# Kernel tuning notes

Hardware: AMD Instinct MI355X
Metric: run time of the kernel (lower is better)

The kernel has to match this reference:

```python
import jax, jax.numpy as jnp
import numpy as np

IN_CH = 512
MID_CH = IN_CH // 8  # 64


def setup_inputs() -> dict:
    key = jax.random.key(0)
    ks = jax.random.split(key, 7)
    B, C, H, W = 8, IN_CH, 64, 64
    s = 1.0 / np.sqrt(C)
    x = jax.random.normal(ks[0], (B, C, H, W), dtype=jnp.float32)
    wq = jax.random.normal(ks[1], (MID_CH, C), dtype=jnp.float32) * s
    bq = jax.random.normal(ks[2], (MID_CH,), dtype=jnp.float32) * 0.01
    wk = jax.random.normal(ks[3], (MID_CH, C), dtype=jnp.float32) * s
    bk = jax.random.normal(ks[4], (MID_CH,), dtype=jnp.float32) * 0.01
    wv = jax.random.normal(ks[5], (C, C), dtype=jnp.float32) * s
    bv = jax.random.normal(ks[6], (C,), dtype=jnp.float32) * 0.01
    gamma = jnp.array([0.5], dtype=jnp.float32)
    return {"x": x, "wq": wq, "bq": bq, "wk": wk, "bk": bk,
            "wv": wv, "bv": bv, "gamma": gamma}


def reference(x, wq, bq, wk, bk, wv, bv, gamma):
    B, C, H, W = x.shape
    N = H * W
    xf = x.reshape(B, C, N)  # flatten spatial -> [B, C, N]
    # 1x1 convs are channel-wise matmuls
    q = jnp.einsum('mc,bcn->bnm', wq, xf) + bq  # [B, N, mid]
    k = jnp.einsum('mc,bcn->bmn', wk, xf) + bk[None, :, None]  # [B, mid, N]
    v = jnp.einsum('oc,bcn->bon', wv, xf) + bv[None, :, None]  # [B, C, N]
    sim = jnp.einsum('bnm,bmj->bnj', q, k)  # [B, N, N]
    sim = jax.nn.softmax(sim, axis=-1)
    # feat[b,c,i] = sum_j v[b,c,j] * sim[b,i,j]   (value @ sim^T)
    feat = jnp.einsum('bcj,bij->bci', v, sim).reshape(B, C, H, W)
    return gamma[0] * feat + x
```

## Files before the change

kernel.cpp:

```cpp
#include <hip/hip_runtime.h>
#include <hip/hip_bf16.h>


#define BB 8
#define CC 512
#define MM 64
#define NN 4096
#define LOG2E 1.4426950408889634f

typedef __attribute__((ext_vector_type(8))) short bf16x8;
typedef __attribute__((ext_vector_type(8))) _Float16 f16x8;
typedef __attribute__((ext_vector_type(4))) float f32x4;

__device__ unsigned g_kmax[BB];

__device__ __forceinline__ unsigned short f2bf(float f) {
  union { float f; unsigned u; } v; v.f = f;
  unsigned r = v.u + 0x7fffu + ((v.u >> 16) & 1u);
  return (unsigned short)(r >> 16);
}
__device__ __forceinline__ float bf2f(unsigned short h) {
  union { unsigned u; float f; } v; v.u = ((unsigned)h) << 16;
  return v.f;
}
__device__ __forceinline__ unsigned short f2h(float f) {
  union { _Float16 h; unsigned short u; } v; v.h = (_Float16)f;
  return v.u;
}

__global__ __launch_bounds__(256) void k_wconv(
    const float* __restrict__ wq, const float* __restrict__ wk,
    const float* __restrict__ wv,
    unsigned short* __restrict__ wqhi, unsigned short* __restrict__ wqlo,
    unsigned short* __restrict__ wkhi, unsigned short* __restrict__ wklo,
    unsigned short* __restrict__ wvbf) {
  const int tid = blockIdx.x * 256 + threadIdx.x;
  if (tid < BB) g_kmax[tid] = 0u;
  if (tid < MM * CC) {
    float v = wq[tid];
    unsigned short h = f2bf(v);
    wqhi[tid] = h; wqlo[tid] = f2bf(v - bf2f(h));
    v = wk[tid]; h = f2bf(v);
    wkhi[tid] = h; wklo[tid] = f2bf(v - bf2f(h));
  }
  for (int i = tid; i < CC * CC; i += 65536) wvbf[i] = f2bf(wv[i]);
}

__global__ __launch_bounds__(256) void k_transpose(const float* __restrict__ x,
                                                   unsigned short* __restrict__ xT) {
  __shared__ float tile[64][65];
  const int b = blockIdx.z, c0 = blockIdx.y * 64, n0 = blockIdx.x * 64;
  const int t = threadIdx.x;
  {
    const int nl = t & 63, cl0 = t >> 6;
    const float* xp = x + ((size_t)b * CC + c0) * NN + n0;
#pragma unroll
    for (int r = 0; r < 16; r++) {
      const int cl = cl0 + r * 4;
      tile[cl][nl] = xp[(size_t)cl * NN + nl];
    }
  }
  __syncthreads();
  {
    const int cl = t & 63, nl0 = t >> 6;
    unsigned short* xtp = xT + ((size_t)b * NN + n0) * CC + c0;
#pragma unroll
    for (int r = 0; r < 16; r++) {
      const int nl = nl0 + r * 4;
      xtp[(size_t)nl * CC + cl] = f2bf(tile[cl][nl]);
    }
  }
}

__global__ __launch_bounds__(256, 2) void k_proj(
    const unsigned short* __restrict__ xT,
    const unsigned short* __restrict__ wqhi, const unsigned short* __restrict__ wqlo,
    const unsigned short* __restrict__ wkhi, const unsigned short* __restrict__ wklo,
    const float* __restrict__ bq, const float* __restrict__ bk,
    const unsigned short* __restrict__ wvbf, const float* __restrict__ bv,
    unsigned short* __restrict__ qf, unsigned short* __restrict__ kf,
    unsigned short* __restrict__ vbf) {
  __shared__ float ksl[4][4][16];
  const int t = threadIdx.x, w = t >> 6, l = t & 63, lr = l & 15, g = l >> 4;

  if (blockIdx.x < 512) {
    const int b = blockIdx.x & 7;
    const int n0 = (blockIdx.x >> 3) * 64;
    const unsigned short* qhp = wqhi + (size_t)(w * 16 + lr) * CC + g * 8;
    const unsigned short* qlp = wqlo + (size_t)(w * 16 + lr) * CC + g * 8;
    const unsigned short* khp = wkhi + (size_t)(w * 16 + lr) * CC + g * 8;
    const unsigned short* klp = wklo + (size_t)(w * 16 + lr) * CC + g * 8;
    const unsigned short* xp = xT + ((size_t)b * NN + n0 + lr) * CC + g * 8;
    f32x4 qacc[4], kacc[4];
#pragma unroll
    for (int nf = 0; nf < 4; nf++) {
      qacc[nf] = f32x4{0.f, 0.f, 0.f, 0.f};
      kacc[nf] = f32x4{0.f, 0.f, 0.f, 0.f};
    }
    for (int cc = 0; cc < CC; cc += 32) {
      const bf16x8 qh8 = *reinterpret_cast<const bf16x8*>(qhp + cc);
      const bf16x8 ql8 = *reinterpret_cast<const bf16x8*>(qlp + cc);
      const bf16x8 kh8 = *reinterpret_cast<const bf16x8*>(khp + cc);
      const bf16x8 kl8 = *reinterpret_cast<const bf16x8*>(klp + cc);
      bf16x8 xb[4];
#pragma unroll
      for (int nf = 0; nf < 4; nf++)
        xb[nf] = *reinterpret_cast<const bf16x8*>(xp + (size_t)nf * 16 * CC + cc);
#pragma unroll
      for (int nf = 0; nf < 4; nf++) {
        qacc[nf] = __builtin_amdgcn_mfma_f32_16x16x32_bf16(qh8, xb[nf], qacc[nf], 0, 0, 0);
        qacc[nf] = __builtin_amdgcn_mfma_f32_16x16x32_bf16(ql8, xb[nf], qacc[nf], 0, 0, 0);
        kacc[nf] = __builtin_amdgcn_mfma_f32_16x16x32_bf16(kh8, xb[nf], kacc[nf], 0, 0, 0);
        kacc[nf] = __builtin_amdgcn_mfma_f32_16x16x32_bf16(kl8, xb[nf], kacc[nf], 0, 0, 0);
      }
    }
    float bqv[4], bkv[4];
#pragma unroll
    for (int r = 0; r < 4; r++) {
      bqv[r] = bq[w * 16 + g * 4 + r];
      bkv[r] = bk[w * 16 + g * 4 + r];
    }
    float kssp[4];
#pragma unroll
    for (int nf = 0; nf < 4; nf++) {
      float ks2 = 0.f;
      unsigned short qh[4], kh[4];
#pragma unroll
      for (int r = 0; r < 4; r++) {
        const float qv = (qacc[nf][r] + bqv[r]) * LOG2E;
        const float kv = kacc[nf][r] + bkv[r];
        qh[r] = f2h(qv); kh[r] = f2h(kv);
        ks2 += kv * kv;
      }
      kssp[nf] = ks2;
      const int n = n0 + nf * 16 + lr;
      const size_t base = ((size_t)b * NN + n) * MM + w * 16 + g * 4;
      *reinterpret_cast<ushort4*>(qf + base) = make_ushort4(qh[0], qh[1], qh[2], qh[3]);
      *reinterpret_cast<ushort4*>(kf + base) = make_ushort4(kh[0], kh[1], kh[2], kh[3]);
    }
#pragma unroll
    for (int nf = 0; nf < 4; nf++) {
      kssp[nf] += __shfl_xor(kssp[nf], 16);
      kssp[nf] += __shfl_xor(kssp[nf], 32);
    }
    if (l < 16) {
#pragma unroll
      for (int nf = 0; nf < 4; nf++) ksl[w][nf][lr] = kssp[nf];
    }
    __syncthreads();
    if (t < 64) {
      const int nf2 = t >> 4, lr2 = t & 15;
      float kn2 = ksl[0][nf2][lr2] + ksl[1][nf2][lr2] + ksl[2][nf2][lr2] + ksl[3][nf2][lr2];
#pragma unroll
      for (int d = 1; d < 64; d <<= 1) kn2 = fmaxf(kn2, __shfl_xor(kn2, d));
      if (t == 0) atomicMax(&g_kmax[b], __float_as_uint(kn2));
    }
  } else {
    const int blk = blockIdx.x - 512;
    const int b = blk >> 8, c0 = ((blk >> 5) & 7) * 64, n0 = (blk & 31) * 128;
    const int nbase = n0 + w * 32;
    f32x4 acc[4][2];
#pragma unroll
    for (int cf = 0; cf < 4; cf++) {
      acc[cf][0] = f32x4{0.f, 0.f, 0.f, 0.f};
      acc[cf][1] = f32x4{0.f, 0.f, 0.f, 0.f};
    }
    for (int ks = 0; ks < 16; ks++) {
      const int kk = ks * 32 + g * 8;
      bf16x8 bfr[2];
#pragma unroll
      for (int nf = 0; nf < 2; nf++) {
        const int n = nbase + nf * 16 + lr;
        bfr[nf] = *reinterpret_cast<const bf16x8*>(xT + ((size_t)b * NN + n) * CC + kk);
      }
#pragma unroll
      for (int cf = 0; cf < 4; cf++) {
        const bf16x8 af = *reinterpret_cast<const bf16x8*>(
            wvbf + (size_t)(c0 + cf * 16 + lr) * CC + kk);
        acc[cf][0] = __builtin_amdgcn_mfma_f32_16x16x32_bf16(af, bfr[0], acc[cf][0], 0, 0, 0);
        acc[cf][1] = __builtin_amdgcn_mfma_f32_16x16x32_bf16(af, bfr[1], acc[cf][1], 0, 0, 0);
      }
    }
#pragma unroll
    for (int cf = 0; cf < 4; cf++) {
#pragma unroll
      for (int r = 0; r < 4; r++) {
        const int c = c0 + cf * 16 + g * 4 + r;
        const float bvv = bv[c];
#pragma unroll
        for (int nf = 0; nf < 2; nf++) {
          const int n = nbase + nf * 16 + lr;
          vbf[((size_t)b * CC + c) * NN + n] = f2bf(acc[cf][nf][r] + bvv);
        }
      }
    }
  }
}

__global__ __launch_bounds__(512, 2) void k_attn(
    const unsigned short* __restrict__ qf, const unsigned short* __restrict__ kf,
    const unsigned short* __restrict__ vbf, const float* __restrict__ x,
    const float* __restrict__ gamma, float* __restrict__ out) {
  __shared__ unsigned short P_lds[2][128][64];
  __shared__ float l_red[8][4][16];
  const int b = blockIdx.x & 7;
  const int idx = blockIdx.x >> 3;
  const int i0 = (idx >> 1) * 128;
  const int ch = idx & 1;
  const int t = threadIdx.x, w = t >> 6, l = t & 63, lr = l & 15, g = l >> 4;
  const int jf = w & 3, ig = w >> 2;
  const int wc = ch * 256 + w * 32;

  f16x8 qF[4][2];
#pragma unroll
  for (int q = 0; q < 4; q++) {
    const int i = i0 + (ig * 4 + q) * 16 + lr;
#pragma unroll
    for (int ks = 0; ks < 2; ks++)
      qF[q][ks] = *reinterpret_cast<const f16x8*>(qf + ((size_t)b * NN + i) * MM + ks * 32 + g * 8);
  }
  float mhat[4];
  {
    const float kroot = sqrtf(__uint_as_float(g_kmax[b])) * 1.001f;
#pragma unroll
    for (int q = 0; q < 4; q++) {
      float ssq = 0.f;
#pragma unroll
      for (int ks = 0; ks < 2; ks++)
#pragma unroll
        for (int e = 0; e < 8; e++) {
          const float qv = (float)qF[q][ks][e];
          ssq += qv * qv;
        }
      ssq += __shfl_xor(ssq, 16);
      ssq += __shfl_xor(ssq, 32);
      mhat[q] = sqrtf(ssq) * kroot - 63.4786f;
    }
  }

  const unsigned short* kp = kf + ((size_t)b * NN + jf * 16 + lr) * MM + g * 8;
  const unsigned short* pv = vbf + ((size_t)b * CC + wc + lr) * NN + g * 8;

  f32x4 acc[2][8];
#pragma unroll
  for (int cf = 0; cf < 2; cf++)
#pragma unroll
    for (int i2 = 0; i2 < 8; i2++) acc[cf][i2] = f32x4{0.f, 0.f, 0.f, 0.f};
  float lsum[4] = {0.f, 0.f, 0.f, 0.f};

  char* const pbase = (char*)&P_lds[0][0][0];
  int off_s[4];
#pragma unroll
  for (int q = 0; q < 4; q++) {
    const int row = (ig * 4 + q) * 16 + lr;
    off_s[q] = (row << 7) + ((jf * 32 + g * 8) ^ ((row & 7) << 4));
  }

  f16x8 kA[2], kB[2];
#pragma unroll
  for (int ks = 0; ks < 2; ks++)
    kA[ks] = *reinterpret_cast<const f16x8*>(kp + (size_t)ks * 32);
  bf16x8 va[2][2], vb[2][2];
#pragma unroll
  for (int ks = 0; ks < 2; ks++)
#pragma unroll
    for (int cf = 0; cf < 2; cf++)
      va[ks][cf] = *reinterpret_cast<const bf16x8*>(pv + (size_t)cf * (16 * NN) + ks * 32);
#pragma unroll
  for (int q = 0; q < 4; q++) {
    f32x4 sa = __builtin_amdgcn_mfma_f32_16x16x32_f16(kA[0], qF[q][0],
                                                      f32x4{0.f, 0.f, 0.f, 0.f}, 0, 0, 0);
    sa = __builtin_amdgcn_mfma_f32_16x16x32_f16(kA[1], qF[q][1], sa, 0, 0, 0);
    const float p0 = __builtin_amdgcn_exp2f(sa[0] - mhat[q]);
    const float p1 = __builtin_amdgcn_exp2f(sa[1] - mhat[q]);
    const float p2 = __builtin_amdgcn_exp2f(sa[2] - mhat[q]);
    const float p3 = __builtin_amdgcn_exp2f(sa[3] - mhat[q]);
    lsum[q] += (p0 + p1) + (p2 + p3);
    unsigned r01, r23;
    asm volatile("v_cvt_pk_bf16_f32 %0, %1, %2" : "=v"(r01) : "v"(p0), "v"(p1));
    asm volatile("v_cvt_pk_bf16_f32 %0, %1, %2" : "=v"(r23) : "v"(p2), "v"(p3));
    *reinterpret_cast<uint2*>(pbase + off_s[q]) = make_uint2(r01, r23);
  }
#pragma unroll
  for (int ks = 0; ks < 2; ks++)
    kB[ks] = *reinterpret_cast<const f16x8*>(kp + (size_t)64 * MM + ks * 32);
  __builtin_amdgcn_sched_barrier(0);
  asm volatile("s_waitcnt lgkmcnt(0)" ::: "memory");
  __builtin_amdgcn_s_barrier();
  __builtin_amdgcn_sched_barrier(0);

  auto region = [&](int jb, bf16x8 (&vcur)[2][2], bf16x8 (&vnext)[2][2],
                    f16x8 (&kuse)[2], f16x8 (&kpre)[2]) {
    const int par = (jb >> 6) & 1;
    const int j1 = (jb + 64) & (NN - 1);
    const int j2 = (jb + 128) & (NN - 1);
#pragma unroll
    for (int ks = 0; ks < 2; ks++)
#pragma unroll
      for (int cf = 0; cf < 2; cf++)
        vnext[ks][cf] = *reinterpret_cast<const bf16x8*>(
            pv + (size_t)cf * (16 * NN) + j1 + ks * 32);
    f32x4 sa[4];
#pragma unroll
    for (int q = 0; q < 4; q++) {
      sa[q] = __builtin_amdgcn_mfma_f32_16x16x32_f16(kuse[0], qF[q][0],
                                                     f32x4{0.f, 0.f, 0.f, 0.f}, 0, 0, 0);
      sa[q] = __builtin_amdgcn_mfma_f32_16x16x32_f16(kuse[1], qF[q][1], sa[q], 0, 0, 0);
    }
#pragma unroll
    for (int ks = 0; ks < 2; ks++)
      kpre[ks] = *reinterpret_cast<const f16x8*>(kp + (size_t)j2 * MM + ks * 32);
    const bool vld = (jb + 64) < NN;
    char* const pw = pbase + ((par ^ 1) << 14);
#pragma unroll
    for (int q = 0; q < 4; q++) {
      const float p0 = __builtin_amdgcn_exp2f(sa[q][0] - mhat[q]);
      const float p1 = __builtin_amdgcn_exp2f(sa[q][1] - mhat[q]);
      const float p2 = __builtin_amdgcn_exp2f(sa[q][2] - mhat[q]);
      const float p3 = __builtin_amdgcn_exp2f(sa[q][3] - mhat[q]);
      if (vld) lsum[q] += (p0 + p1) + (p2 + p3);
      unsigned r01, r23;
      asm volatile("v_cvt_pk_bf16_f32 %0, %1, %2" : "=v"(r01) : "v"(p0), "v"(p1));
      asm volatile("v_cvt_pk_bf16_f32 %0, %1, %2" : "=v"(r23) : "v"(p2), "v"(p3));
      *reinterpret_cast<uint2*>(pw + off_s[q]) = make_uint2(r01, r23);
    }
    char* const pr = pbase + (par << 14);
    __builtin_amdgcn_s_setprio(1);
#pragma unroll
    for (int ks = 0; ks < 2; ks++) {
#pragma unroll
      for (int i2 = 0; i2 < 8; i2++) {
        const int row = i2 * 16 + lr;
        const int colb = ks * 64 + g * 16;
        const bf16x8 pf = *reinterpret_cast<const bf16x8*>(
            pr + (row << 7) + (colb ^ ((row & 7) << 4)));
        acc[0][i2] = __builtin_amdgcn_mfma_f32_16x16x32_bf16(vcur[ks][0], pf, acc[0][i2], 0, 0, 0);
        acc[1][i2] = __builtin_amdgcn_mfma_f32_16x16x32_bf16(vcur[ks][1], pf, acc[1][i2], 0, 0, 0);
      }
    }
    __builtin_amdgcn_s_setprio(0);
    __builtin_amdgcn_sched_barrier(0);
    asm volatile("s_waitcnt lgkmcnt(0)" ::: "memory");
    __builtin_amdgcn_s_barrier();
    __builtin_amdgcn_sched_barrier(0);
  };

  for (int tt = 0; tt < 32; tt++) {
    region(tt * 128, va, vb, kB, kA);
    region(tt * 128 + 64, vb, va, kA, kB);
  }

#pragma unroll
  for (int q = 0; q < 4; q++) {
    lsum[q] += __shfl_xor(lsum[q], 16);
    lsum[q] += __shfl_xor(lsum[q], 32);
  }
  __syncthreads();
  if (l < 16) {
#pragma unroll
    for (int q = 0; q < 4; q++) l_red[w][q][lr] = lsum[q];
  }
  __syncthreads();
  const float gm = gamma[0];
  float inv[8];
#pragma unroll
  for (int i2 = 0; i2 < 8; i2++) {
    const int ig2 = i2 >> 2, q = i2 & 3;
    inv[i2] = gm / (l_red[ig2 * 4 + 0][q][lr] + l_red[ig2 * 4 + 1][q][lr] +
                    l_red[ig2 * 4 + 2][q][lr] + l_red[ig2 * 4 + 3][q][lr]);
  }

#pragma unroll
  for (int cf = 0; cf < 2; cf++) {
#pragma unroll
    for (int r = 0; r < 4; r++) {
      const int c = wc + cf * 16 + g * 4 + r;
      const size_t rowo = ((size_t)b * CC + c) * NN;
#pragma unroll
      for (int i2 = 0; i2 < 8; i2++) {
        const int i = i0 + i2 * 16 + lr;
        out[rowo + i] = acc[cf][i2][r] * inv[i2] + x[rowo + i];
      }
    }
  }
}

extern "C" void kernel_launch(void* const* d_in, const int* in_sizes, int n_in,
                              void* d_out, int out_size, void* d_ws, size_t ws_size,
                              hipStream_t stream) {
  const float* x = (const float*)d_in[0];
  const float* wq = (const float*)d_in[1];
  const float* bq = (const float*)d_in[2];
  const float* wk = (const float*)d_in[3];
  const float* bk = (const float*)d_in[4];
  const float* wv = (const float*)d_in[5];
  const float* bv = (const float*)d_in[6];
  const float* gamma = (const float*)d_in[7];
  float* out = (float*)d_out;

  char* ws = (char*)d_ws;
  unsigned short* xT = (unsigned short*)(ws);
  unsigned short* vbf = (unsigned short*)(ws + 33554432);
  unsigned short* qfp = (unsigned short*)(ws + 67108864);
  unsigned short* kfp = (unsigned short*)(ws + 71303168);
  unsigned short* wqhi = (unsigned short*)(ws + 75497472);
  unsigned short* wqlo = (unsigned short*)(ws + 75563008);
  unsigned short* wkhi = (unsigned short*)(ws + 75628544);
  unsigned short* wklo = (unsigned short*)(ws + 75694080);
  unsigned short* wvbf = (unsigned short*)(ws + 75759616);

  k_wconv<<<256, 256, 0, stream>>>(wq, wk, wv, wqhi, wqlo, wkhi, wklo, wvbf);
  k_transpose<<<dim3(64, 8, 8), 256, 0, stream>>>(x, xT);
  k_proj<<<2560, 256, 0, stream>>>(xT, wqhi, wqlo, wkhi, wklo, bq, bk, wvbf, bv,
                                   qfp, kfp, vbf);
  k_attn<<<dim3(512), 512, 0, stream>>>(qfp, kfp, vbf, x, gamma, out);
}
```

Measured before the change: 335.6 us.

## Halve attention query tile, raise occupancy, widen V-proj tile, vectorize transpose

The attention kernel now processes 64 query rows per block instead of 128, launching twice as many blocks with launch bounds allowing 4 blocks per CU. The work is re-split so each wave computes scores for one 16-row query group against 32 keys. The V register double-buffer is dropped in favour of loads inside each region. The V projection now uses 64x256 tiles per block with 4x4 MFMA accumulators, and the x transpose uses float4 loads and ushort4 stores. The aim is better latency hiding and fewer memory transactions, at the cost of reading K and V twice as often per query row and exposing V load latency within each region.

```diff
diff --git a/kernel.cpp b/kernel.cpp
--- a/kernel.cpp
+++ b/kernel.cpp
@@ -52,22 +52,26 @@
   const int b = blockIdx.z, c0 = blockIdx.y * 64, n0 = blockIdx.x * 64;
   const int t = threadIdx.x;
   {
-    const int nl = t & 63, cl0 = t >> 6;
+    const int nq = (t & 15) * 4, cl0 = t >> 4;
     const float* xp = x + ((size_t)b * CC + c0) * NN + n0;
 #pragma unroll
-    for (int r = 0; r < 16; r++) {
-      const int cl = cl0 + r * 4;
-      tile[cl][nl] = xp[(size_t)cl * NN + nl];
+    for (int r = 0; r < 4; r++) {
+      const int row = cl0 + r * 16;
+      const f32x4 v = *reinterpret_cast<const f32x4*>(xp + (size_t)row * NN + nq);
+      tile[row][nq] = v[0]; tile[row][nq + 1] = v[1];
+      tile[row][nq + 2] = v[2]; tile[row][nq + 3] = v[3];
     }
   }
   __syncthreads();
   {
-    const int cl = t & 63, nl0 = t >> 6;
+    const int cq = (t & 15) * 4, nl0 = t >> 4;
     unsigned short* xtp = xT + ((size_t)b * NN + n0) * CC + c0;
 #pragma unroll
-    for (int r = 0; r < 16; r++) {
-      const int nl = nl0 + r * 4;
-      xtp[(size_t)nl * CC + cl] = f2bf(tile[cl][nl]);
+    for (int r = 0; r < 4; r++) {
+      const int n = nl0 + r * 16;
+      const ushort4 o = make_ushort4(f2bf(tile[cq][n]), f2bf(tile[cq + 1][n]),
+                                     f2bf(tile[cq + 2][n]), f2bf(tile[cq + 3][n]));
+      *reinterpret_cast<ushort4*>(xtp + (size_t)n * CC + cq) = o;
     }
   }
 }
@@ -157,19 +161,18 @@
     }
   } else {
     const int blk = blockIdx.x - 512;
-    const int b = blk >> 8, c0 = ((blk >> 5) & 7) * 64, n0 = (blk & 31) * 128;
-    const int nbase = n0 + w * 32;
-    f32x4 acc[4][2];
-#pragma unroll
-    for (int cf = 0; cf < 4; cf++) {
-      acc[cf][0] = f32x4{0.f, 0.f, 0.f, 0.f};
-      acc[cf][1] = f32x4{0.f, 0.f, 0.f, 0.f};
-    }
+    const int b = blk >> 7, c0 = ((blk >> 4) & 7) * 64, n0 = (blk & 15) * 256;
+    const int nbase = n0 + w * 64;
+    f32x4 acc[4][4];
+#pragma unroll
+    for (int cf = 0; cf < 4; cf++)
+#pragma unroll
+      for (int nf = 0; nf < 4; nf++) acc[cf][nf] = f32x4{0.f, 0.f, 0.f, 0.f};
     for (int ks = 0; ks < 16; ks++) {
       const int kk = ks * 32 + g * 8;
-      bf16x8 bfr[2];
-#pragma unroll
-      for (int nf = 0; nf < 2; nf++) {
+      bf16x8 bfr[4];
+#pragma unroll
+      for (int nf = 0; nf < 4; nf++) {
         const int n = nbase + nf * 16 + lr;
         bfr[nf] = *reinterpret_cast<const bf16x8*>(xT + ((size_t)b * NN + n) * CC + kk);
       }
@@ -177,8 +180,9 @@
       for (int cf = 0; cf < 4; cf++) {
         const bf16x8 af = *reinterpret_cast<const bf16x8*>(
             wvbf + (size_t)(c0 + cf * 16 + lr) * CC + kk);
-        acc[cf][0] = __builtin_amdgcn_mfma_f32_16x16x32_bf16(af, bfr[0], acc[cf][0], 0, 0, 0);
-        acc[cf][1] = __builtin_amdgcn_mfma_f32_16x16x32_bf16(af, bfr[1], acc[cf][1], 0, 0, 0);
+#pragma unroll
+        for (int nf = 0; nf < 4; nf++)
+          acc[cf][nf] = __builtin_amdgcn_mfma_f32_16x16x32_bf16(af, bfr[nf], acc[cf][nf], 0, 0, 0);
       }
     }
 #pragma unroll
@@ -188,7 +192,7 @@
         const int c = c0 + cf * 16 + g * 4 + r;
         const float bvv = bv[c];
 #pragma unroll
-        for (int nf = 0; nf < 2; nf++) {
+        for (int nf = 0; nf < 4; nf++) {
           const int n = nbase + nf * 16 + lr;
           vbf[((size_t)b * CC + c) * NN + n] = f2bf(acc[cf][nf][r] + bvv);
         }
@@ -197,145 +201,141 @@
   }
 }
 
-__global__ __launch_bounds__(512, 2) void k_attn(
+__global__ __launch_bounds__(512, 4) void k_attn(
     const unsigned short* __restrict__ qf, const unsigned short* __restrict__ kf,
     const unsigned short* __restrict__ vbf, const float* __restrict__ x,
     const float* __restrict__ gamma, float* __restrict__ out) {
-  __shared__ unsigned short P_lds[2][128][64];
-  __shared__ float l_red[8][4][16];
+  __shared__ unsigned short P_lds[2][64][64];
+  __shared__ float l_red[8][16];
   const int b = blockIdx.x & 7;
   const int idx = blockIdx.x >> 3;
-  const int i0 = (idx >> 1) * 128;
+  const int i0 = (idx >> 1) * 64;
   const int ch = idx & 1;
   const int t = threadIdx.x, w = t >> 6, l = t & 63, lr = l & 15, g = l >> 4;
-  const int jf = w & 3, ig = w >> 2;
+  const int if_ = w & 3;
+  const int jp = w >> 2;
   const int wc = ch * 256 + w * 32;
 
-  f16x8 qF[4][2];
-#pragma unroll
-  for (int q = 0; q < 4; q++) {
-    const int i = i0 + (ig * 4 + q) * 16 + lr;
+  f16x8 qF[2];
+  {
+    const int i = i0 + if_ * 16 + lr;
 #pragma unroll
     for (int ks = 0; ks < 2; ks++)
-      qF[q][ks] = *reinterpret_cast<const f16x8*>(qf + ((size_t)b * NN + i) * MM + ks * 32 + g * 8);
-  }
-  float mhat[4];
+      qF[ks] = *reinterpret_cast<const f16x8*>(qf + ((size_t)b * NN + i) * MM + ks * 32 + g * 8);
+  }
+  float mhat;
   {
-    const float kroot = sqrtf(__uint_as_float(g_kmax[b])) * 1.001f;
-#pragma unroll
-    for (int q = 0; q < 4; q++) {
-      float ssq = 0.f;
-#pragma unroll
-      for (int ks = 0; ks < 2; ks++)
-#pragma unroll
-        for (int e = 0; e < 8; e++) {
-          const float qv = (float)qF[q][ks][e];
-          ssq += qv * qv;
-        }
-      ssq += __shfl_xor(ssq, 16);
-      ssq += __shfl_xor(ssq, 32);
-      mhat[q] = sqrtf(ssq) * kroot - 63.4786f;
-    }
-  }
-
-  const unsigned short* kp = kf + ((size_t)b * NN + jf * 16 + lr) * MM + g * 8;
+    float ssq = 0.f;
+#pragma unroll
+    for (int ks = 0; ks < 2; ks++)
+#pragma unroll
+      for (int e = 0; e < 8; e++) {
+        const float qv = (float)qF[ks][e];
+        ssq += qv * qv;
+      }
+    ssq += __shfl_xor(ssq, 16);
+    ssq += __shfl_xor(ssq, 32);
+    mhat = sqrtf(ssq) * sqrtf(__uint_as_float(g_kmax[b])) * 1.001f - 63.4786f;
+  }
+
+  const unsigned short* kp = kf + ((size_t)b * NN + jp * 32 + lr) * MM + g * 8;
   const unsigned short* pv = vbf + ((size_t)b * CC + wc + lr) * NN + g * 8;
 
-  f32x4 acc[2][8];
+  f32x4 acc[2][4];
 #pragma unroll
   for (int cf = 0; cf < 2; cf++)
 #pragma unroll
-    for (int i2 = 0; i2 < 8; i2++) acc[cf][i2] = f32x4{0.f, 0.f, 0.f, 0.f};
-  float lsum[4] = {0.f, 0.f, 0.f, 0.f};
+    for (int i2 = 0; i2 < 4; i2++) acc[cf][i2] = f32x4{0.f, 0.f, 0.f, 0.f};
+  float lsum = 0.f;
 
   char* const pbase = (char*)&P_lds[0][0][0];
-  int off_s[4];
-#pragma unroll
-  for (int q = 0; q < 4; q++) {
-    const int row = (ig * 4 + q) * 16 + lr;
-    off_s[q] = (row << 7) + ((jf * 32 + g * 8) ^ ((row & 7) << 4));
-  }
-
-  f16x8 kA[2], kB[2];
-#pragma unroll
-  for (int ks = 0; ks < 2; ks++)
-    kA[ks] = *reinterpret_cast<const f16x8*>(kp + (size_t)ks * 32);
-  bf16x8 va[2][2], vb[2][2];
-#pragma unroll
-  for (int ks = 0; ks < 2; ks++)
-#pragma unroll
-    for (int cf = 0; cf < 2; cf++)
-      va[ks][cf] = *reinterpret_cast<const bf16x8*>(pv + (size_t)cf * (16 * NN) + ks * 32);
-#pragma unroll
-  for (int q = 0; q < 4; q++) {
-    f32x4 sa = __builtin_amdgcn_mfma_f32_16x16x32_f16(kA[0], qF[q][0],
+  int off_s[2];
+#pragma unroll
+  for (int jf = 0; jf < 2; jf++) {
+    const int row = if_ * 16 + lr;
+    off_s[jf] = (row << 7) + (((jp * 2 + jf) * 32 + g * 8) ^ ((row & 7) << 4));
+  }
+
+  f16x8 kA[2][2], kB[2][2];
+#pragma unroll
+  for (int jf = 0; jf < 2; jf++)
+#pragma unroll
+    for (int ks = 0; ks < 2; ks++)
+      kA[jf][ks] = *reinterpret_cast<const f16x8*>(kp + (size_t)(jf * 16) * MM + ks * 32);
+#pragma unroll
+  for (int jf = 0; jf < 2; jf++) {
+    f32x4 sa = __builtin_amdgcn_mfma_f32_16x16x32_f16(kA[jf][0], qF[0],
                                                       f32x4{0.f, 0.f, 0.f, 0.f}, 0, 0, 0);
-    sa = __builtin_amdgcn_mfma_f32_16x16x32_f16(kA[1], qF[q][1], sa, 0, 0, 0);
-    const float p0 = __builtin_amdgcn_exp2f(sa[0] - mhat[q]);
-    const float p1 = __builtin_amdgcn_exp2f(sa[1] - mhat[q]);
-    const float p2 = __builtin_amdgcn_exp2f(sa[2] - mhat[q]);
-    const float p3 = __builtin_amdgcn_exp2f(sa[3] - mhat[q]);
-    lsum[q] += (p0 + p1) + (p2 + p3);
+    sa = __builtin_amdgcn_mfma_f32_16x16x32_f16(kA[jf][1], qF[1], sa, 0, 0, 0);
+    const float p0 = __builtin_amdgcn_exp2f(sa[0] - mhat);
+    const float p1 = __builtin_amdgcn_exp2f(sa[1] - mhat);
+    const float p2 = __builtin_amdgcn_exp2f(sa[2] - mhat);
+    const float p3 = __builtin_amdgcn_exp2f(sa[3] - mhat);
+    lsum += (p0 + p1) + (p2 + p3);
     unsigned r01, r23;
     asm volatile("v_cvt_pk_bf16_f32 %0, %1, %2" : "=v"(r01) : "v"(p0), "v"(p1));
     asm volatile("v_cvt_pk_bf16_f32 %0, %1, %2" : "=v"(r23) : "v"(p2), "v"(p3));
-    *reinterpret_cast<uint2*>(pbase + off_s[q]) = make_uint2(r01, r23);
-  }
-#pragma unroll
-  for (int ks = 0; ks < 2; ks++)
-    kB[ks] = *reinterpret_cast<const f16x8*>(kp + (size_t)64 * MM + ks * 32);
+    *reinterpret_cast<uint2*>(pbase + off_s[jf]) = make_uint2(r01, r23);
+  }
+#pragma unroll
+  for (int jf = 0; jf < 2; jf++)
+#pragma unroll
+    for (int ks = 0; ks < 2; ks++)
+      kB[jf][ks] = *reinterpret_cast<const f16x8*>(kp + (size_t)(64 + jf * 16) * MM + ks * 32);
   __builtin_amdgcn_sched_barrier(0);
   asm volatile("s_waitcnt lgkmcnt(0)" ::: "memory");
   __builtin_amdgcn_s_barrier();
   __builtin_amdgcn_sched_barrier(0);
 
-  auto region = [&](int jb, bf16x8 (&vcur)[2][2], bf16x8 (&vnext)[2][2],
-                    f16x8 (&kuse)[2], f16x8 (&kpre)[2]) {
+  auto region = [&](int jb, f16x8 (&kuse)[2][2], f16x8 (&kpre)[2][2]) {
     const int par = (jb >> 6) & 1;
-    const int j1 = (jb + 64) & (NN - 1);
     const int j2 = (jb + 128) & (NN - 1);
+    bf16x8 vr[2][2];
 #pragma unroll
     for (int ks = 0; ks < 2; ks++)
 #pragma unroll
       for (int cf = 0; cf < 2; cf++)
-        vnext[ks][cf] = *reinterpret_cast<const bf16x8*>(
-            pv + (size_t)cf * (16 * NN) + j1 + ks * 32);
-    f32x4 sa[4];
-#pragma unroll
-    for (int q = 0; q < 4; q++) {
-      sa[q] = __builtin_amdgcn_mfma_f32_16x16x32_f16(kuse[0], qF[q][0],
-                                                     f32x4{0.f, 0.f, 0.f, 0.f}, 0, 0, 0);
-      sa[q] = __builtin_amdgcn_mfma_f32_16x16x32_f16(kuse[1], qF[q][1], sa[q], 0, 0, 0);
-    }
-#pragma unroll
-    for (int ks = 0; ks < 2; ks++)
-      kpre[ks] = *reinterpret_cast<const f16x8*>(kp + (size_t)j2 * MM + ks * 32);
+        vr[ks][cf] = *reinterpret_cast<const bf16x8*>(
+            pv + (size_t)cf * (16 * NN) + jb + ks * 32);
+    f32x4 sa[2];
+#pragma unroll
+    for (int jf = 0; jf < 2; jf++) {
+      sa[jf] = __builtin_amdgcn_mfma_f32_16x16x32_f16(kuse[jf][0], qF[0],
+                                                      f32x4{0.f, 0.f, 0.f, 0.f}, 0, 0, 0);
+      sa[jf] = __builtin_amdgcn_mfma_f32_16x16x32_f16(kuse[jf][1], qF[1], sa[jf], 0, 0, 0);
+    }
+#pragma unroll
+    for (int jf = 0; jf < 2; jf++)
+#pragma unroll
+      for (int ks = 0; ks < 2; ks++)
+        kpre[jf][ks] = *reinterpret_cast<const f16x8*>(
+            kp + (size_t)(j2 + jf * 16) * MM + ks * 32);
     const bool vld = (jb + 64) < NN;
-    char* const pw = pbase + ((par ^ 1) << 14);
-#pragma unroll
-    for (int q = 0; q < 4; q++) {
-      const float p0 = __builtin_amdgcn_exp2f(sa[q][0] - mhat[q]);
-      const float p1 = __builtin_amdgcn_exp2f(sa[q][1] - mhat[q]);
-      const float p2 = __builtin_amdgcn_exp2f(sa[q][2] - mhat[q]);
-      const float p3 = __builtin_amdgcn_exp2f(sa[q][3] - mhat[q]);
-      if (vld) lsum[q] += (p0 + p1) + (p2 + p3);
+    char* const pw = pbase + ((par ^ 1) << 13);
+#pragma unroll
+    for (int jf = 0; jf < 2; jf++) {
+      const float p0 = __builtin_amdgcn_exp2f(sa[jf][0] - mhat);
+      const float p1 = __builtin_amdgcn_exp2f(sa[jf][1] - mhat);
+      const float p2 = __builtin_amdgcn_exp2f(sa[jf][2] - mhat);
+      const float p3 = __builtin_amdgcn_exp2f(sa[jf][3] - mhat);
+      if (vld) lsum += (p0 + p1) + (p2 + p3);
       unsigned r01, r23;
       asm volatile("v_cvt_pk_bf16_f32 %0, %1, %2" : "=v"(r01) : "v"(p0), "v"(p1));
       asm volatile("v_cvt_pk_bf16_f32 %0, %1, %2" : "=v"(r23) : "v"(p2), "v"(p3));
-      *reinterpret_cast<uint2*>(pw + off_s[q]) = make_uint2(r01, r23);
-    }
-    char* const pr = pbase + (par << 14);
+      *reinterpret_cast<uint2*>(pw + off_s[jf]) = make_uint2(r01, r23);
+    }
+    char* const pr = pbase + (par << 13);
     __builtin_amdgcn_s_setprio(1);
 #pragma unroll
     for (int ks = 0; ks < 2; ks++) {
 #pragma unroll
-      for (int i2 = 0; i2 < 8; i2++) {
+      for (int i2 = 0; i2 < 4; i2++) {
         const int row = i2 * 16 + lr;
         const int colb = ks * 64 + g * 16;
         const bf16x8 pf = *reinterpret_cast<const bf16x8*>(
             pr + (row << 7) + (colb ^ ((row & 7) << 4)));
-        acc[0][i2] = __builtin_amdgcn_mfma_f32_16x16x32_bf16(vcur[ks][0], pf, acc[0][i2], 0, 0, 0);
-        acc[1][i2] = __builtin_amdgcn_mfma_f32_16x16x32_bf16(vcur[ks][1], pf, acc[1][i2], 0, 0, 0);
+        acc[0][i2] = __builtin_amdgcn_mfma_f32_16x16x32_bf16(vr[ks][0], pf, acc[0][i2], 0, 0, 0);
+        acc[1][i2] = __builtin_amdgcn_mfma_f32_16x16x32_bf16(vr[ks][1], pf, acc[1][i2], 0, 0, 0);
       }
     }
     __builtin_amdgcn_s_setprio(0);
@@ -346,29 +346,18 @@
   };
 
   for (int tt = 0; tt < 32; tt++) {
-    region(tt * 128, va, vb, kB, kA);
-    region(tt * 128 + 64, vb, va, kA, kB);
-  }
-
-#pragma unroll
-  for (int q = 0; q < 4; q++) {
-    lsum[q] += __shfl_xor(lsum[q], 16);
-    lsum[q] += __shfl_xor(lsum[q], 32);
-  }
-  __syncthreads();
-  if (l < 16) {
-#pragma unroll
-    for (int q = 0; q < 4; q++) l_red[w][q][lr] = lsum[q];
-  }
+    region(tt * 128, kB, kA);
+    region(tt * 128 + 64, kA, kB);
+  }
+
+  lsum += __shfl_xor(lsum, 16);
+  lsum += __shfl_xor(lsum, 32);
+  if (l < 16) l_red[w][lr] = lsum;
   __syncthreads();
   const float gm = gamma[0];
-  float inv[8];
-#pragma unroll
-  for (int i2 = 0; i2 < 8; i2++) {
-    const int ig2 = i2 >> 2, q = i2 & 3;
-    inv[i2] = gm / (l_red[ig2 * 4 + 0][q][lr] + l_red[ig2 * 4 + 1][q][lr] +
-                    l_red[ig2 * 4 + 2][q][lr] + l_red[ig2 * 4 + 3][q][lr]);
-  }
+  float inv[4];
+#pragma unroll
+  for (int i2 = 0; i2 < 4; i2++) inv[i2] = gm / (l_red[i2][lr] + l_red[i2 + 4][lr]);
 
 #pragma unroll
   for (int cf = 0; cf < 2; cf++) {
@@ -377,7 +366,7 @@
       const int c = wc + cf * 16 + g * 4 + r;
       const size_t rowo = ((size_t)b * CC + c) * NN;
 #pragma unroll
-      for (int i2 = 0; i2 < 8; i2++) {
+      for (int i2 = 0; i2 < 4; i2++) {
         const int i = i0 + i2 * 16 + lr;
         out[rowo + i] = acc[cf][i2][r] * inv[i2] + x[rowo + i];
       }
@@ -411,7 +400,7 @@
 
   k_wconv<<<256, 256, 0, stream>>>(wq, wk, wv, wqhi, wqlo, wkhi, wklo, wvbf);
   k_transpose<<<dim3(64, 8, 8), 256, 0, stream>>>(x, xT);
-  k_proj<<<2560, 256, 0, stream>>>(xT, wqhi, wqlo, wkhi, wklo, bq, bk, wvbf, bv,
+  k_proj<<<1536, 256, 0, stream>>>(xT, wqhi, wqlo, wkhi, wklo, bq, bk, wvbf, bv,
                                    qfp, kfp, vbf);
-  k_attn<<<dim3(512), 512, 0, stream>>>(qfp, kfp, vbf, x, gamma, out);
-}
+  k_attn<<<dim3(1024), 512, 0, stream>>>(qfp, kfp, vbf, x, gamma, out);
+}
```

Measured after the change: 585.1 us. +74.3%, slower.
